# Kernel tuning notes

Hardware: AMD Instinct MI355X
Metric: run time of the kernel (lower is better)

The kernel has to match this reference:

```python
import jax, jax.numpy as jnp
import numpy as np

NUM_HEADS = 4
HEAD_DIM = 64  # hidden_dim // num_heads = 256 // 4
NEG_SLOPE = 0.2


def setup_inputs() -> dict:
    key0 = jax.random.key(0)
    ks = jax.random.split(key0, 8)
    B, N, QD, VD = 32, 8192, 256, 256
    HD = NUM_HEADS * HEAD_DIM  # 256
    s_in = 1.0 / np.sqrt(QD)
    s_v = 1.0 / np.sqrt(VD)
    s_a = 1.0 / np.sqrt(HEAD_DIM)
    return {
        "query": jax.random.normal(ks[0], (B, QD), jnp.float32),
        "key": jax.random.normal(ks[1], (B, N, QD), jnp.float32),
        "value": jax.random.normal(ks[2], (B, N, VD), jnp.float32),
        # linear_query == linear_key (shared_weights=True)
        "Wq": jax.random.uniform(ks[3], (QD, HD), jnp.float32, -s_in, s_in),
        "bq": jax.random.uniform(ks[4], (HD,), jnp.float32, -s_in, s_in),
        # node_projection
        "Wv": jax.random.uniform(ks[5], (VD, HD), jnp.float32, -s_v, s_v),
        "bv": jax.random.uniform(ks[6], (HD,), jnp.float32, -s_v, s_v),
        # attention: Linear(head_dim, 1, bias=False)
        "a": jax.random.uniform(ks[7], (HEAD_DIM,), jnp.float32, -s_a, s_a),
    }


def reference(query, key, value, Wq, bq, Wv, bv, a):
    B, N, _ = key.shape
    H, D = NUM_HEADS, HEAD_DIM
    # projections (shared query/key weights)
    hq = (query @ Wq + bq).reshape(B, 1, H, D)          # [B,1,H,D]
    hk = (key @ Wq + bq).reshape(B, N, H, D)            # [B,N,H,D]
    hv = (value @ Wv + bv).reshape(B, N, H, D)          # [B,N,H,D]
    # additive attention score: leaky_relu(broadcast add) projected to scalar per head
    e = jax.nn.leaky_relu(hq + hk, negative_slope=NEG_SLOPE)  # [B,N,H,D]
    e = jnp.einsum('bnhd,d->bnh', e, a)                 # [B,N,H]
    # dropout=0.0 (eval) -> identity; softmax over nodes
    e = jax.nn.softmax(e, axis=1)                       # [B,N,H]
    scored = jnp.einsum('bnh,bnhf->bhf', e, hv)         # [B,H,D]
    h_prime = jax.nn.relu(scored.reshape(B, H * D))     # [B,H*D] (is_concat)
    return h_prime, e
```

## Files before the change

kernel.cpp:

```cpp
#include <hip/hip_runtime.h>
#include <hip/hip_bf16.h>

#define NUM_HEADS 4
#define HD 256
#define QD 256
#define VD 256
#define B_SZ 32
#define N_NODES 8192
#define NEG_SLOPE 0.2f
#define CH 16
#define NCH 32
#define KSTRIDE 1040

typedef short bf16x8 __attribute__((ext_vector_type(8)));
typedef float f32x4 __attribute__((ext_vector_type(4)));

static __device__ __forceinline__ unsigned short f2bf(float f) {
    __hip_bfloat16 h = __float2bfloat16(f);
    return *reinterpret_cast<unsigned short*>(&h);
}

static __device__ __forceinline__ void gload_lds16(const float* g, void* l) {
    __builtin_amdgcn_global_load_lds(
        (const __attribute__((address_space(1))) void*)g,
        (__attribute__((address_space(3))) void*)l, 16, 0, 0);
}

__global__ __launch_bounds__(256)
void prep_kernel(const float* __restrict__ query,
                 const float* __restrict__ Wq,
                 const float* __restrict__ bq,
                 unsigned short* __restrict__ WqP,
                 float* __restrict__ hqb) {
    int blk = blockIdx.x;
    int tid = threadIdx.x;
    if (blk < 32) {
        int b = blk, col = tid;
        float acc = 2.0f * bq[col];
#pragma unroll 16
        for (int k = 0; k < QD; ++k)
            acc += query[b * QD + k] * Wq[k * HD + col];
        hqb[b * HD + col] = acc;
    } else {
        int idx = blk - 32;
        int kstep = idx >> 2, g = idx & 3;
        int col = tid;
        int h = col >> 6, ct = (col >> 4) & 3, col16 = col & 15;
        unsigned short v[8];
#pragma unroll
        for (int j = 0; j < 8; ++j)
            v[j] = f2bf(Wq[(kstep * 32 + g * 8 + j) * HD + col]);
        *reinterpret_cast<uint4*>(
            WqP + kstep * 8192 + h * 2048 + ct * 512 + (g * 16 + col16) * 8) =
            *reinterpret_cast<uint4*>(v);
    }
}

__global__ __launch_bounds__(256, 2)
void fused_kernel(const float* __restrict__ key,
                  const float* __restrict__ value,
                  const unsigned short* __restrict__ WqP,
                  const float* __restrict__ hqb,
                  const float* __restrict__ avec,
                  float* __restrict__ s,
                  float* __restrict__ p_part,
                  float* __restrict__ pml) {
    __shared__ __align__(16) char smem[2 * (CH * KSTRIDE) + 2 * (CH * 1024)];

    char* kb0 = smem;
    char* kb1 = smem + CH * KSTRIDE;
    char* vb0 = smem + 2 * CH * KSTRIDE;
    char* vb1 = vb0 + CH * 1024;

    int bid = blockIdx.x;
    int b = bid >> 4, strip = bid & 15;
    int tid = threadIdx.x;
    int w = tid >> 6, lane = tid & 63;
    int col16 = lane & 15, g = (lane >> 4) & 3;
    int h = w;
    int rowbase0 = strip * 512;

    bf16x8 bfr[8][4];
    {
        const unsigned short* wp0 = WqP + h * 2048 + (g * 16 + col16) * 8;
#pragma unroll
        for (int ks = 0; ks < 8; ++ks)
#pragma unroll
            for (int ct = 0; ct < 4; ++ct)
                bfr[ks][ct] = *reinterpret_cast<const bf16x8*>(wp0 + ks * 8192 + ct * 512);
    }
    float av16[4][4], hq16[4][4];
#pragma unroll
    for (int ct = 0; ct < 4; ++ct)
#pragma unroll
        for (int r = 0; r < 4; ++r) {
            int d = ct * 16 + g * 4 + r;
            av16[ct][r] = avec[d];
            hq16[ct][r] = hqb[b * HD + h * 64 + d];
        }

    float mr = -1e30f, lr = 0.f;
    f32x4 pa = (f32x4){0.f, 0.f, 0.f, 0.f};

    {
        int rb = rowbase0;
#pragma unroll
        for (int r = 0; r < 4; ++r) {
            int lr_ = w * 4 + r;
            gload_lds16(key + ((size_t)(b * N_NODES + rb + lr_)) * QD + lane * 4,
                        kb0 + lr_ * KSTRIDE);
        }
#pragma unroll
        for (int r = 0; r < 4; ++r) {
            int lr_ = w * 4 + r;
            gload_lds16(value + ((size_t)(b * N_NODES + rb + lr_)) * VD + lane * 4,
                        vb0 + lr_ * 1024);
        }
    }

    for (int t = 0; t < NCH; ++t) {
        __builtin_amdgcn_s_barrier();
        if (t + 1 < NCH) {
            char* kbn = ((t + 1) & 1) ? kb1 : kb0;
            char* vbn = ((t + 1) & 1) ? vb1 : vb0;
            int rb = rowbase0 + (t + 1) * CH;
#pragma unroll
            for (int r = 0; r < 4; ++r) {
                int lr_ = w * 4 + r;
                gload_lds16(key + ((size_t)(b * N_NODES + rb + lr_)) * QD + lane * 4,
                            kbn + lr_ * KSTRIDE);
            }
#pragma unroll
            for (int r = 0; r < 4; ++r) {
                int lr_ = w * 4 + r;
                gload_lds16(value + ((size_t)(b * N_NODES + rb + lr_)) * VD + lane * 4,
                            vbn + lr_ * 1024);
            }
            asm volatile("s_waitcnt vmcnt(8)" ::: "memory");
        } else {
            asm volatile("s_waitcnt vmcnt(0)" ::: "memory");
        }
        __builtin_amdgcn_s_barrier();
        __builtin_amdgcn_sched_barrier(0);

        const char* kb = (t & 1) ? kb1 : kb0;
        const char* vb = (t & 1) ? vb1 : vb0;
        int n0c = rowbase0 + t * CH;

        bf16x8 a[8];
#pragma unroll
        for (int ks = 0; ks < 8; ++ks) {
            f32x4 lo = *reinterpret_cast<const f32x4*>(kb + col16 * KSTRIDE + ks * 128 + g * 32);
            f32x4 hi = *reinterpret_cast<const f32x4*>(kb + col16 * KSTRIDE + ks * 128 + g * 32 + 16);
            unsigned int u0, u1, u2, u3;
            asm("v_cvt_pk_bf16_f32 %0, %1, %2" : "=v"(u0) : "v"(lo[0]), "v"(lo[1]));
            asm("v_cvt_pk_bf16_f32 %0, %1, %2" : "=v"(u1) : "v"(lo[2]), "v"(lo[3]));
            asm("v_cvt_pk_bf16_f32 %0, %1, %2" : "=v"(u2) : "v"(hi[0]), "v"(hi[1]));
            asm("v_cvt_pk_bf16_f32 %0, %1, %2" : "=v"(u3) : "v"(hi[2]), "v"(hi[3]));
            uint4 tt = {u0, u1, u2, u3};
            a[ks] = *reinterpret_cast<bf16x8*>(&tt);
        }

        f32x4 acc[4];
#pragma unroll
        for (int ct = 0; ct < 4; ++ct) acc[ct] = (f32x4){0.f, 0.f, 0.f, 0.f};
#pragma unroll
        for (int ks = 0; ks < 8; ++ks)
#pragma unroll
            for (int ct = 0; ct < 4; ++ct)
                acc[ct] = __builtin_amdgcn_mfma_f32_16x16x32_bf16(bfr[ks][ct], a[ks], acc[ct], 0, 0, 0);

        float dot = 0.f;
#pragma unroll
        for (int ct = 0; ct < 4; ++ct) {
#pragma unroll
            for (int r = 0; r < 4; ++r) {
                float pre = acc[ct][r] + hq16[ct][r];
                float tv = fmaxf(pre, NEG_SLOPE * pre);
                dot += av16[ct][r] * tv;
            }
        }
        dot += __shfl_xor(dot, 16, 64);
        dot += __shfl_xor(dot, 32, 64);

        if (lane < 16) {
            s[((size_t)(b * NUM_HEADS + h)) * N_NODES + n0c + lane] = dot;
        }

        float mc = dot;
        mc = fmaxf(mc, __shfl_xor(mc, 1, 64));
        mc = fmaxf(mc, __shfl_xor(mc, 2, 64));
        mc = fmaxf(mc, __shfl_xor(mc, 4, 64));
        mc = fmaxf(mc, __shfl_xor(mc, 8, 64));
        float mnew = fmaxf(mr, mc);
        float ep = __expf(dot - mnew);
        float lc = ep;
        lc += __shfl_xor(lc, 1, 64);
        lc += __shfl_xor(lc, 2, 64);
        lc += __shfl_xor(lc, 4, 64);
        lc += __shfl_xor(lc, 8, 64);
        float scf = __expf(mr - mnew);
        pa *= scf;
        lr = lr * scf + lc;
        mr = mnew;

#pragma unroll
        for (int n = 0; n < 16; ++n) {
            f32x4 v = *reinterpret_cast<const f32x4*>(vb + n * 1024 + lane * 16);
            float e = __shfl(ep, n, 64);
            pa += e * v;
        }
    }

    int slot = bid * 4 + w;
    *reinterpret_cast<f32x4*>(p_part + (size_t)slot * 256 + lane * 4) = pa;
    if (lane == 0) {
        pml[slot * 2] = mr;
        pml[slot * 2 + 1] = lr;
    }
}

__global__ __launch_bounds__(256)
void final_kernel(const float* __restrict__ p_part,
                  const float* __restrict__ pml,
                  const float* __restrict__ Wv,
                  const float* __restrict__ bv,
                  float* __restrict__ hout,
                  float* __restrict__ sc) {
    int bh = blockIdx.x;
    int b = bh >> 2, h = bh & 3;
    int tid = threadIdx.x;

    int slots[16];
    float mv[16], lv[16];
    float M = -1e30f;
#pragma unroll
    for (int i = 0; i < 16; ++i) {
        slots[i] = (b * 16 + i) * 4 + h;
        mv[i] = pml[slots[i] * 2];
        lv[i] = pml[slots[i] * 2 + 1];
        M = fmaxf(M, mv[i]);
    }
    float L = 0.f, acc = 0.f;
#pragma unroll
    for (int i = 0; i < 16; ++i) {
        float wf = __expf(mv[i] - M);
        L += wf * lv[i];
        acc += wf * p_part[(size_t)slots[i] * 256 + tid];
    }
    float invL = 1.0f / L;
    if (tid == 0) {
        sc[bh * 2] = M;
        sc[bh * 2 + 1] = invL;
    }
    __shared__ float ps[256];
    ps[tid] = acc * invL;
    __syncthreads();

    int d = tid & 63, kr = tid >> 6;
    float a2 = 0.f;
#pragma unroll 8
    for (int k = kr * 64; k < kr * 64 + 64; ++k)
        a2 += ps[k] * Wv[k * HD + h * 64 + d];
    __shared__ float rs[4][64];
    rs[kr][d] = a2;
    __syncthreads();
    if (tid < 64) {
        float o = bv[h * 64 + tid] + rs[0][tid] + rs[1][tid] + rs[2][tid] + rs[3][tid];
        hout[b * HD + h * 64 + tid] = fmaxf(o, 0.f);
    }
}

__global__ __launch_bounds__(256)
void epass_kernel(const float* __restrict__ s,
                  const float* __restrict__ sc,
                  float* __restrict__ e_out) {
    int bid = blockIdx.x;
    int b = bid >> 5, t = bid & 31;
    int n = t * 256 + threadIdx.x;
    float4 ev;
#pragma unroll
    for (int h = 0; h < 4; ++h) {
        float M = sc[(b * 4 + h) * 2];
        float invL = sc[(b * 4 + h) * 2 + 1];
        float sv = s[((size_t)(b * 4 + h)) * N_NODES + n];
        (&ev.x)[h] = __expf(sv - M) * invL;
    }
    *reinterpret_cast<float4*>(e_out + ((size_t)(b * N_NODES + n)) * 4) = ev;
}

extern "C" void kernel_launch(void* const* d_in, const int* in_sizes, int n_in,
                              void* d_out, int out_size, void* d_ws, size_t ws_size,
                              hipStream_t stream) {
    const float* query = (const float*)d_in[0];
    const float* key   = (const float*)d_in[1];
    const float* value = (const float*)d_in[2];
    const float* Wq    = (const float*)d_in[3];
    const float* bq    = (const float*)d_in[4];
    const float* Wv    = (const float*)d_in[5];
    const float* bv    = (const float*)d_in[6];
    const float* avec  = (const float*)d_in[7];
    float* out = (float*)d_out;

    char* ws = (char*)d_ws;
    unsigned short* WqP = (unsigned short*)ws;
    float* hqb    = (float*)(ws + 131072);
    float* s      = (float*)(ws + 163840);
    float* pml    = (float*)(ws + 4358144);
    float* sc     = (float*)(ws + 4374528);
    float* p_part = (float*)(ws + 4378624);

    prep_kernel<<<64, 256, 0, stream>>>(query, Wq, bq, WqP, hqb);
    fused_kernel<<<512, 256, 0, stream>>>(key, value, WqP, hqb, avec, s, p_part, pml);
    final_kernel<<<B_SZ * NUM_HEADS, 256, 0, stream>>>(p_part, pml, Wv, bv, out, sc);
    epass_kernel<<<B_SZ * 32, 256, 0, stream>>>(s, sc, out + B_SZ * HD);
}
```

Measured before the change: 132.3 us.

## Warp-specialize fused kernel with producer loaders and 3-slot LDS ring

The fused kernel now runs 512 threads per block. Four producer waves stream key/value chunks into a 3-slot shared-memory ring, and four consumer waves (one per head) do the MFMA score and online-softmax accumulation. Handoff uses LDS flag counters with atomics and spin-sleep instead of block-wide barriers. Each block covers 1024 nodes, so half as many blocks launch and the final reduction merges 8 partials instead of 16. The goal is to overlap global loads with compute more deeply. The cost is fewer blocks, spin-wait overhead, and the risk that flag ordering bugs produce hazards.

After: 187.4 us. 41.6% more time.

```diff
diff --git a/kernel.cpp b/kernel.cpp
--- a/kernel.cpp
+++ b/kernel.cpp
@@ -9,8 +9,10 @@
 #define N_NODES 8192
 #define NEG_SLOPE 0.2f
 #define CH 16
-#define NCH 32
+#define NCH 64
 #define KSTRIDE 1040
+#define RING 3
+#define SLOT (CH * KSTRIDE + CH * 1024)
 
 typedef short bf16x8 __attribute__((ext_vector_type(8)));
 typedef float f32x4 __attribute__((ext_vector_type(4)));
@@ -56,7 +58,7 @@
     }
 }
 
-__global__ __launch_bounds__(256, 2)
+__global__ __launch_bounds__(512, 2)
 void fused_kernel(const float* __restrict__ key,
                   const float* __restrict__ value,
                   const unsigned short* __restrict__ WqP,
@@ -65,158 +67,154 @@
                   float* __restrict__ s,
                   float* __restrict__ p_part,
                   float* __restrict__ pml) {
-    __shared__ __align__(16) char smem[2 * (CH * KSTRIDE) + 2 * (CH * 1024)];
-
-    char* kb0 = smem;
-    char* kb1 = smem + CH * KSTRIDE;
-    char* vb0 = smem + 2 * CH * KSTRIDE;
-    char* vb1 = vb0 + CH * 1024;
+    __shared__ __align__(16) char smem[RING * SLOT + 64];
+    int* flags = reinterpret_cast<int*>(smem + RING * SLOT);
+    volatile int* vflags = flags;
 
     int bid = blockIdx.x;
-    int b = bid >> 4, strip = bid & 15;
+    int b = bid >> 3, strip = bid & 7;
     int tid = threadIdx.x;
     int w = tid >> 6, lane = tid & 63;
-    int col16 = lane & 15, g = (lane >> 4) & 3;
-    int h = w;
-    int rowbase0 = strip * 512;
-
-    bf16x8 bfr[8][4];
-    {
-        const unsigned short* wp0 = WqP + h * 2048 + (g * 16 + col16) * 8;
-#pragma unroll
-        for (int ks = 0; ks < 8; ++ks)
-#pragma unroll
-            for (int ct = 0; ct < 4; ++ct)
-                bfr[ks][ct] = *reinterpret_cast<const bf16x8*>(wp0 + ks * 8192 + ct * 512);
-    }
-    float av16[4][4], hq16[4][4];
-#pragma unroll
-    for (int ct = 0; ct < 4; ++ct)
-#pragma unroll
-        for (int r = 0; r < 4; ++r) {
-            int d = ct * 16 + g * 4 + r;
-            av16[ct][r] = avec[d];
-            hq16[ct][r] = hqb[b * HD + h * 64 + d];
-        }
-
-    float mr = -1e30f, lr = 0.f;
-    f32x4 pa = (f32x4){0.f, 0.f, 0.f, 0.f};
-
-    {
-        int rb = rowbase0;
-#pragma unroll
-        for (int r = 0; r < 4; ++r) {
-            int lr_ = w * 4 + r;
-            gload_lds16(key + ((size_t)(b * N_NODES + rb + lr_)) * QD + lane * 4,
-                        kb0 + lr_ * KSTRIDE);
-        }
-#pragma unroll
-        for (int r = 0; r < 4; ++r) {
-            int lr_ = w * 4 + r;
-            gload_lds16(value + ((size_t)(b * N_NODES + rb + lr_)) * VD + lane * 4,
-                        vb0 + lr_ * 1024);
-        }
-    }
-
-    for (int t = 0; t < NCH; ++t) {
-        __builtin_amdgcn_s_barrier();
-        if (t + 1 < NCH) {
-            char* kbn = ((t + 1) & 1) ? kb1 : kb0;
-            char* vbn = ((t + 1) & 1) ? vb1 : vb0;
-            int rb = rowbase0 + (t + 1) * CH;
+    int rowbase0 = strip * 1024;
+
+    if (tid < 2 * RING) flags[tid] = (tid < RING) ? 0 : 4;
+    __syncthreads();
+
+    if (w < 4) {
+        for (int t = 0; t < NCH; ++t) {
+            int sl = t % RING, e = t / RING;
+            while (vflags[RING + sl] < 4 * e + 4) __builtin_amdgcn_s_sleep(2);
+            char* kslot = smem + sl * SLOT;
+            char* vslot = kslot + CH * KSTRIDE;
+            int rb = rowbase0 + t * CH;
 #pragma unroll
             for (int r = 0; r < 4; ++r) {
                 int lr_ = w * 4 + r;
                 gload_lds16(key + ((size_t)(b * N_NODES + rb + lr_)) * QD + lane * 4,
-                            kbn + lr_ * KSTRIDE);
+                            kslot + lr_ * KSTRIDE);
             }
 #pragma unroll
             for (int r = 0; r < 4; ++r) {
                 int lr_ = w * 4 + r;
                 gload_lds16(value + ((size_t)(b * N_NODES + rb + lr_)) * VD + lane * 4,
-                            vbn + lr_ * 1024);
-            }
-            asm volatile("s_waitcnt vmcnt(8)" ::: "memory");
-        } else {
-            asm volatile("s_waitcnt vmcnt(0)" ::: "memory");
+                            vslot + lr_ * 1024);
+            }
+            if (t > 0) {
+                asm volatile("s_waitcnt vmcnt(8)" ::: "memory");
+                if (lane == 0) atomicAdd(&flags[(t - 1) % RING], 1);
+            }
         }
-        __builtin_amdgcn_s_barrier();
-        __builtin_amdgcn_sched_barrier(0);
-
-        const char* kb = (t & 1) ? kb1 : kb0;
-        const char* vb = (t & 1) ? vb1 : vb0;
-        int n0c = rowbase0 + t * CH;
-
-        bf16x8 a[8];
-#pragma unroll
-        for (int ks = 0; ks < 8; ++ks) {
-            f32x4 lo = *reinterpret_cast<const f32x4*>(kb + col16 * KSTRIDE + ks * 128 + g * 32);
-            f32x4 hi = *reinterpret_cast<const f32x4*>(kb + col16 * KSTRIDE + ks * 128 + g * 32 + 16);
-            unsigned int u0, u1, u2, u3;
-            asm("v_cvt_pk_bf16_f32 %0, %1, %2" : "=v"(u0) : "v"(lo[0]), "v"(lo[1]));
-            asm("v_cvt_pk_bf16_f32 %0, %1, %2" : "=v"(u1) : "v"(lo[2]), "v"(lo[3]));
-            asm("v_cvt_pk_bf16_f32 %0, %1, %2" : "=v"(u2) : "v"(hi[0]), "v"(hi[1]));
-            asm("v_cvt_pk_bf16_f32 %0, %1, %2" : "=v"(u3) : "v"(hi[2]), "v"(hi[3]));
-            uint4 tt = {u0, u1, u2, u3};
-            a[ks] = *reinterpret_cast<bf16x8*>(&tt);
+        asm volatile("s_waitcnt vmcnt(0)" ::: "memory");
+        if (lane == 0) atomicAdd(&flags[(NCH - 1) % RING], 1);
+    } else {
+        int h = w - 4;
+        int col16 = lane & 15, g = (lane >> 4) & 3;
+
+        bf16x8 bfr[8][4];
+        {
+            const unsigned short* wp0 = WqP + h * 2048 + (g * 16 + col16) * 8;
+#pragma unroll
+            for (int ks = 0; ks < 8; ++ks)
+#pragma unroll
+                for (int ct = 0; ct < 4; ++ct)
+                    bfr[ks][ct] = *reinterpret_cast<const bf16x8*>(wp0 + ks * 8192 + ct * 512);
         }
-
-        f32x4 acc[4];
-#pragma unroll
-        for (int ct = 0; ct < 4; ++ct) acc[ct] = (f32x4){0.f, 0.f, 0.f, 0.f};
-#pragma unroll
-        for (int ks = 0; ks < 8; ++ks)
-#pragma unroll
-            for (int ct = 0; ct < 4; ++ct)
-                acc[ct] = __builtin_amdgcn_mfma_f32_16x16x32_bf16(bfr[ks][ct], a[ks], acc[ct], 0, 0, 0);
-
-        float dot = 0.f;
-#pragma unroll
-        for (int ct = 0; ct < 4; ++ct) {
+        float av16[4][4], hq16[4][4];
+#pragma unroll
+        for (int ct = 0; ct < 4; ++ct)
 #pragma unroll
             for (int r = 0; r < 4; ++r) {
-                float pre = acc[ct][r] + hq16[ct][r];
-                float tv = fmaxf(pre, NEG_SLOPE * pre);
-                dot += av16[ct][r] * tv;
-            }
+                int d = ct * 16 + g * 4 + r;
+                av16[ct][r] = avec[d];
+                hq16[ct][r] = hqb[b * HD + h * 64 + d];
+            }
+
+        float mr = -1e30f, lr = 0.f;
+        f32x4 pa = (f32x4){0.f, 0.f, 0.f, 0.f};
+
+        for (int t = 0; t < NCH; ++t) {
+            int sl = t % RING, e = t / RING;
+            while (vflags[sl] < 4 * (e + 1)) __builtin_amdgcn_s_sleep(2);
+            asm volatile("s_waitcnt lgkmcnt(0)" ::: "memory");
+            __builtin_amdgcn_sched_barrier(0);
+
+            const char* kb = smem + sl * SLOT;
+            const char* vb = kb + CH * KSTRIDE;
+            int n0c = rowbase0 + t * CH;
+
+            bf16x8 a[8];
+#pragma unroll
+            for (int ks = 0; ks < 8; ++ks) {
+                f32x4 lo = *reinterpret_cast<const f32x4*>(kb + col16 * KSTRIDE + ks * 128 + g * 32);
+                f32x4 hi = *reinterpret_cast<const f32x4*>(kb + col16 * KSTRIDE + ks * 128 + g * 32 + 16);
+                unsigned int u0, u1, u2, u3;
+                asm("v_cvt_pk_bf16_f32 %0, %1, %2" : "=v"(u0) : "v"(lo[0]), "v"(lo[1]));
+                asm("v_cvt_pk_bf16_f32 %0, %1, %2" : "=v"(u1) : "v"(lo[2]), "v"(lo[3]));
+                asm("v_cvt_pk_bf16_f32 %0, %1, %2" : "=v"(u2) : "v"(hi[0]), "v"(hi[1]));
+                asm("v_cvt_pk_bf16_f32 %0, %1, %2" : "=v"(u3) : "v"(hi[2]), "v"(hi[3]));
+                uint4 tt = {u0, u1, u2, u3};
+                a[ks] = *reinterpret_cast<bf16x8*>(&tt);
+            }
+
+            f32x4 acc[4];
+#pragma unroll
+            for (int ct = 0; ct < 4; ++ct) acc[ct] = (f32x4){0.f, 0.f, 0.f, 0.f};
+#pragma unroll
+            for (int ks = 0; ks < 8; ++ks)
+#pragma unroll
+                for (int ct = 0; ct < 4; ++ct)
+                    acc[ct] = __builtin_amdgcn_mfma_f32_16x16x32_bf16(bfr[ks][ct], a[ks], acc[ct], 0, 0, 0);
+
+            float dot = 0.f;
+#pragma unroll
+            for (int ct = 0; ct < 4; ++ct) {
+#pragma unroll
+                for (int r = 0; r < 4; ++r) {
+                    float pre = acc[ct][r] + hq16[ct][r];
+                    float tv = fmaxf(pre, NEG_SLOPE * pre);
+                    dot += av16[ct][r] * tv;
+                }
+            }
+            dot += __shfl_xor(dot, 16, 64);
+            dot += __shfl_xor(dot, 32, 64);
+
+            if (lane < 16)
+                s[((size_t)(b * NUM_HEADS + h)) * N_NODES + n0c + lane] = dot;
+
+            float mc = dot;
+            mc = fmaxf(mc, __shfl_xor(mc, 1, 64));
+            mc = fmaxf(mc, __shfl_xor(mc, 2, 64));
+            mc = fmaxf(mc, __shfl_xor(mc, 4, 64));
+            mc = fmaxf(mc, __shfl_xor(mc, 8, 64));
+            float mnew = fmaxf(mr, mc);
+            float ep = __expf(dot - mnew);
+            float lc = ep;
+            lc += __shfl_xor(lc, 1, 64);
+            lc += __shfl_xor(lc, 2, 64);
+            lc += __shfl_xor(lc, 4, 64);
+            lc += __shfl_xor(lc, 8, 64);
+            float scf = __expf(mr - mnew);
+            pa *= scf;
+            lr = lr * scf + lc;
+            mr = mnew;
+
+#pragma unroll
+            for (int n = 0; n < 16; ++n) {
+                f32x4 v = *reinterpret_cast<const f32x4*>(vb + n * 1024 + lane * 16);
+                float e2 = __shfl(ep, n, 64);
+                pa += e2 * v;
+            }
+
+            asm volatile("s_waitcnt lgkmcnt(0)" ::: "memory");
+            if (lane == 0) atomicAdd(&flags[RING + sl], 1);
         }
-        dot += __shfl_xor(dot, 16, 64);
-        dot += __shfl_xor(dot, 32, 64);
-
-        if (lane < 16) {
-            s[((size_t)(b * NUM_HEADS + h)) * N_NODES + n0c + lane] = dot;
+
+        int slot = bid * 4 + h;
+        *reinterpret_cast<f32x4*>(p_part + (size_t)slot * 256 + lane * 4) = pa;
+        if (lane == 0) {
+            pml[slot * 2] = mr;
+            pml[slot * 2 + 1] = lr;
         }
-
-        float mc = dot;
-        mc = fmaxf(mc, __shfl_xor(mc, 1, 64));
-        mc = fmaxf(mc, __shfl_xor(mc, 2, 64));
-        mc = fmaxf(mc, __shfl_xor(mc, 4, 64));
-        mc = fmaxf(mc, __shfl_xor(mc, 8, 64));
-        float mnew = fmaxf(mr, mc);
-        float ep = __expf(dot - mnew);
-        float lc = ep;
-        lc += __shfl_xor(lc, 1, 64);
-        lc += __shfl_xor(lc, 2, 64);
-        lc += __shfl_xor(lc, 4, 64);
-        lc += __shfl_xor(lc, 8, 64);
-        float scf = __expf(mr - mnew);
-        pa *= scf;
-        lr = lr * scf + lc;
-        mr = mnew;
-
-#pragma unroll
-        for (int n = 0; n < 16; ++n) {
-            f32x4 v = *reinterpret_cast<const f32x4*>(vb + n * 1024 + lane * 16);
-            float e = __shfl(ep, n, 64);
-            pa += e * v;
-        }
-    }
-
-    int slot = bid * 4 + w;
-    *reinterpret_cast<f32x4*>(p_part + (size_t)slot * 256 + lane * 4) = pa;
-    if (lane == 0) {
-        pml[slot * 2] = mr;
-        pml[slot * 2 + 1] = lr;
     }
 }
 
@@ -231,19 +229,19 @@
     int b = bh >> 2, h = bh & 3;
     int tid = threadIdx.x;
 
-    int slots[16];
-    float mv[16], lv[16];
+    int slots[8];
+    float mv[8], lv[8];
     float M = -1e30f;
 #pragma unroll
-    for (int i = 0; i < 16; ++i) {
-        slots[i] = (b * 16 + i) * 4 + h;
+    for (int i = 0; i < 8; ++i) {
+        slots[i] = (b * 8 + i) * 4 + h;
         mv[i] = pml[slots[i] * 2];
         lv[i] = pml[slots[i] * 2 + 1];
         M = fmaxf(M, mv[i]);
     }
     float L = 0.f, acc = 0.f;
 #pragma unroll
-    for (int i = 0; i < 16; ++i) {
+    for (int i = 0; i < 8; ++i) {
         float wf = __expf(mv[i] - M);
         L += wf * lv[i];
         acc += wf * p_part[(size_t)slots[i] * 256 + tid];
@@ -307,11 +305,11 @@
     float* hqb    = (float*)(ws + 131072);
     float* s      = (float*)(ws + 163840);
     float* pml    = (float*)(ws + 4358144);
-    float* sc     = (float*)(ws + 4374528);
-    float* p_part = (float*)(ws + 4378624);
+    float* sc     = (float*)(ws + 4390912);
+    float* p_part = (float*)(ws + 4395008);
 
     prep_kernel<<<64, 256, 0, stream>>>(query, Wq, bq, WqP, hqb);
-    fused_kernel<<<512, 256, 0, stream>>>(key, value, WqP, hqb, avec, s, p_part, pml);
+    fused_kernel<<<256, 512, 0, stream>>>(key, value, WqP, hqb, avec, s, p_part, pml);
     final_kernel<<<B_SZ * NUM_HEADS, 256, 0, stream>>>(p_part, pml, Wv, bv, out, sc);
     epass_kernel<<<B_SZ * 32, 256, 0, stream>>>(s, sc, out + B_SZ * HD);
 }
```

## Split each head's columns across two waves using 512-thread blocks

Applied to the files above, without the earlier changes.

Fused kernel now launches 512 threads per block, with 8 waves. Each head's 64 output columns are split across two waves, and each wave also takes half of the 16 rows in the value accumulation. Partial scores are combined through a small shared buffer with an extra __syncthreads per chunk. The final kernel now merges 32 partial softmax states per (batch, head) instead of 16. The aim is more waves in flight and fewer registers per wave to better hide memory latency, at the cost of an extra block barrier per chunk and twice as many partials.

New measurement: 235.1 us. 77.6% more time.

```diff
diff --git a/kernel.cpp b/kernel.cpp
--- a/kernel.cpp
+++ b/kernel.cpp
@@ -56,7 +56,7 @@
     }
 }
 
-__global__ __launch_bounds__(256, 2)
+__global__ __launch_bounds__(512, 4)
 void fused_kernel(const float* __restrict__ key,
                   const float* __restrict__ value,
                   const unsigned short* __restrict__ WqP,
@@ -65,38 +65,38 @@
                   float* __restrict__ s,
                   float* __restrict__ p_part,
                   float* __restrict__ pml) {
-    __shared__ __align__(16) char smem[2 * (CH * KSTRIDE) + 2 * (CH * 1024)];
-
+    __shared__ __align__(16) char smem[2 * (CH * KSTRIDE) + 2 * (CH * 1024) + 512];
     char* kb0 = smem;
     char* kb1 = smem + CH * KSTRIDE;
     char* vb0 = smem + 2 * CH * KSTRIDE;
     char* vb1 = vb0 + CH * 1024;
+    float (*xbuf)[2][16] = reinterpret_cast<float(*)[2][16]>(vb1 + CH * 1024);
 
     int bid = blockIdx.x;
     int b = bid >> 4, strip = bid & 15;
     int tid = threadIdx.x;
     int w = tid >> 6, lane = tid & 63;
     int col16 = lane & 15, g = (lane >> 4) & 3;
-    int h = w;
+    int h = w & 3, cth = w >> 2;
     int rowbase0 = strip * 512;
 
-    bf16x8 bfr[8][4];
+    bf16x8 bfr[8][2];
     {
-        const unsigned short* wp0 = WqP + h * 2048 + (g * 16 + col16) * 8;
+        const unsigned short* wp0 = WqP + h * 2048 + cth * 1024 + (g * 16 + col16) * 8;
 #pragma unroll
         for (int ks = 0; ks < 8; ++ks)
 #pragma unroll
-            for (int ct = 0; ct < 4; ++ct)
-                bfr[ks][ct] = *reinterpret_cast<const bf16x8*>(wp0 + ks * 8192 + ct * 512);
-    }
-    float av16[4][4], hq16[4][4];
-#pragma unroll
-    for (int ct = 0; ct < 4; ++ct)
+            for (int ctl = 0; ctl < 2; ++ctl)
+                bfr[ks][ctl] = *reinterpret_cast<const bf16x8*>(wp0 + ks * 8192 + ctl * 512);
+    }
+    float av8[2][4], hq8[2][4];
+#pragma unroll
+    for (int ctl = 0; ctl < 2; ++ctl)
 #pragma unroll
         for (int r = 0; r < 4; ++r) {
-            int d = ct * 16 + g * 4 + r;
-            av16[ct][r] = avec[d];
-            hq16[ct][r] = hqb[b * HD + h * 64 + d];
+            int d = (cth * 2 + ctl) * 16 + g * 4 + r;
+            av8[ctl][r] = avec[d];
+            hq8[ctl][r] = hqb[b * HD + h * 64 + d];
         }
 
     float mr = -1e30f, lr = 0.f;
@@ -105,14 +105,10 @@
     {
         int rb = rowbase0;
 #pragma unroll
-        for (int r = 0; r < 4; ++r) {
-            int lr_ = w * 4 + r;
+        for (int r = 0; r < 2; ++r) {
+            int lr_ = w * 2 + r;
             gload_lds16(key + ((size_t)(b * N_NODES + rb + lr_)) * QD + lane * 4,
                         kb0 + lr_ * KSTRIDE);
-        }
-#pragma unroll
-        for (int r = 0; r < 4; ++r) {
-            int lr_ = w * 4 + r;
             gload_lds16(value + ((size_t)(b * N_NODES + rb + lr_)) * VD + lane * 4,
                         vb0 + lr_ * 1024);
         }
@@ -125,18 +121,18 @@
             char* vbn = ((t + 1) & 1) ? vb1 : vb0;
             int rb = rowbase0 + (t + 1) * CH;
 #pragma unroll
-            for (int r = 0; r < 4; ++r) {
-                int lr_ = w * 4 + r;
+            for (int r = 0; r < 2; ++r) {
+                int lr_ = w * 2 + r;
                 gload_lds16(key + ((size_t)(b * N_NODES + rb + lr_)) * QD + lane * 4,
                             kbn + lr_ * KSTRIDE);
             }
 #pragma unroll
-            for (int r = 0; r < 4; ++r) {
-                int lr_ = w * 4 + r;
+            for (int r = 0; r < 2; ++r) {
+                int lr_ = w * 2 + r;
                 gload_lds16(value + ((size_t)(b * N_NODES + rb + lr_)) * VD + lane * 4,
                             vbn + lr_ * 1024);
             }
-            asm volatile("s_waitcnt vmcnt(8)" ::: "memory");
+            asm volatile("s_waitcnt vmcnt(4)" ::: "memory");
         } else {
             asm volatile("s_waitcnt vmcnt(0)" ::: "memory");
         }
@@ -147,53 +143,60 @@
         const char* vb = (t & 1) ? vb1 : vb0;
         int n0c = rowbase0 + t * CH;
 
-        bf16x8 a[8];
-#pragma unroll
-        for (int ks = 0; ks < 8; ++ks) {
-            f32x4 lo = *reinterpret_cast<const f32x4*>(kb + col16 * KSTRIDE + ks * 128 + g * 32);
-            f32x4 hi = *reinterpret_cast<const f32x4*>(kb + col16 * KSTRIDE + ks * 128 + g * 32 + 16);
-            unsigned int u0, u1, u2, u3;
-            asm("v_cvt_pk_bf16_f32 %0, %1, %2" : "=v"(u0) : "v"(lo[0]), "v"(lo[1]));
-            asm("v_cvt_pk_bf16_f32 %0, %1, %2" : "=v"(u1) : "v"(lo[2]), "v"(lo[3]));
-            asm("v_cvt_pk_bf16_f32 %0, %1, %2" : "=v"(u2) : "v"(hi[0]), "v"(hi[1]));
-            asm("v_cvt_pk_bf16_f32 %0, %1, %2" : "=v"(u3) : "v"(hi[2]), "v"(hi[3]));
-            uint4 tt = {u0, u1, u2, u3};
-            a[ks] = *reinterpret_cast<bf16x8*>(&tt);
-        }
-
-        f32x4 acc[4];
-#pragma unroll
-        for (int ct = 0; ct < 4; ++ct) acc[ct] = (f32x4){0.f, 0.f, 0.f, 0.f};
-#pragma unroll
-        for (int ks = 0; ks < 8; ++ks)
-#pragma unroll
-            for (int ct = 0; ct < 4; ++ct)
-                acc[ct] = __builtin_amdgcn_mfma_f32_16x16x32_bf16(bfr[ks][ct], a[ks], acc[ct], 0, 0, 0);
-
-        float dot = 0.f;
-#pragma unroll
-        for (int ct = 0; ct < 4; ++ct) {
+        f32x4 acc[2];
+        acc[0] = (f32x4){0.f, 0.f, 0.f, 0.f};
+        acc[1] = acc[0];
+#pragma unroll
+        for (int kh = 0; kh < 2; ++kh) {
+            bf16x8 a[4];
+#pragma unroll
+            for (int k2 = 0; k2 < 4; ++k2) {
+                int ks = kh * 4 + k2;
+                f32x4 lo = *reinterpret_cast<const f32x4*>(kb + col16 * KSTRIDE + ks * 128 + g * 32);
+                f32x4 hi = *reinterpret_cast<const f32x4*>(kb + col16 * KSTRIDE + ks * 128 + g * 32 + 16);
+                unsigned int u0, u1, u2, u3;
+                asm("v_cvt_pk_bf16_f32 %0, %1, %2" : "=v"(u0) : "v"(lo[0]), "v"(lo[1]));
+                asm("v_cvt_pk_bf16_f32 %0, %1, %2" : "=v"(u1) : "v"(lo[2]), "v"(lo[3]));
+                asm("v_cvt_pk_bf16_f32 %0, %1, %2" : "=v"(u2) : "v"(hi[0]), "v"(hi[1]));
+                asm("v_cvt_pk_bf16_f32 %0, %1, %2" : "=v"(u3) : "v"(hi[2]), "v"(hi[3]));
+                uint4 tt = {u0, u1, u2, u3};
+                a[k2] = *reinterpret_cast<bf16x8*>(&tt);
+            }
+#pragma unroll
+            for (int k2 = 0; k2 < 4; ++k2)
+#pragma unroll
+                for (int ctl = 0; ctl < 2; ++ctl)
+                    acc[ctl] = __builtin_amdgcn_mfma_f32_16x16x32_bf16(
+                        bfr[kh * 4 + k2][ctl], a[k2], acc[ctl], 0, 0, 0);
+        }
+
+        float dp = 0.f;
+#pragma unroll
+        for (int ctl = 0; ctl < 2; ++ctl)
 #pragma unroll
             for (int r = 0; r < 4; ++r) {
-                float pre = acc[ct][r] + hq16[ct][r];
+                float pre = acc[ctl][r] + hq8[ctl][r];
                 float tv = fmaxf(pre, NEG_SLOPE * pre);
-                dot += av16[ct][r] * tv;
+                dp += av8[ctl][r] * tv;
             }
-        }
-        dot += __shfl_xor(dot, 16, 64);
-        dot += __shfl_xor(dot, 32, 64);
-
-        if (lane < 16) {
-            s[((size_t)(b * NUM_HEADS + h)) * N_NODES + n0c + lane] = dot;
-        }
-
-        float mc = dot;
+        dp += __shfl_xor(dp, 16, 64);
+        dp += __shfl_xor(dp, 32, 64);
+
+        if (lane < 16) xbuf[h][cth][col16] = dp;
+        __syncthreads();
+        float pfull = dp + xbuf[h][1 - cth][col16];
+
+        if (cth == 0 && lane < 16)
+            s[((size_t)(b * NUM_HEADS + h)) * N_NODES + n0c + lane] = pfull;
+
+        float mydot = ((col16 >> 3) == cth) ? pfull : -1e30f;
+        float mc = mydot;
         mc = fmaxf(mc, __shfl_xor(mc, 1, 64));
         mc = fmaxf(mc, __shfl_xor(mc, 2, 64));
         mc = fmaxf(mc, __shfl_xor(mc, 4, 64));
         mc = fmaxf(mc, __shfl_xor(mc, 8, 64));
         float mnew = fmaxf(mr, mc);
-        float ep = __expf(dot - mnew);
+        float ep = __expf(mydot - mnew);
         float lc = ep;
         lc += __shfl_xor(lc, 1, 64);
         lc += __shfl_xor(lc, 2, 64);
@@ -205,14 +208,15 @@
         mr = mnew;
 
 #pragma unroll
-        for (int n = 0; n < 16; ++n) {
-            f32x4 v = *reinterpret_cast<const f32x4*>(vb + n * 1024 + lane * 16);
-            float e = __shfl(ep, n, 64);
+        for (int n = 0; n < 8; ++n) {
+            int row = cth * 8 + n;
+            f32x4 v = *reinterpret_cast<const f32x4*>(vb + row * 1024 + lane * 16);
+            float e = __shfl(ep, row, 64);
             pa += e * v;
         }
     }
 
-    int slot = bid * 4 + w;
+    int slot = bid * 8 + cth * 4 + h;
     *reinterpret_cast<f32x4*>(p_part + (size_t)slot * 256 + lane * 4) = pa;
     if (lane == 0) {
         pml[slot * 2] = mr;
@@ -231,22 +235,19 @@
     int b = bh >> 2, h = bh & 3;
     int tid = threadIdx.x;
 
-    int slots[16];
-    float mv[16], lv[16];
     float M = -1e30f;
-#pragma unroll
-    for (int i = 0; i < 16; ++i) {
-        slots[i] = (b * 16 + i) * 4 + h;
-        mv[i] = pml[slots[i] * 2];
-        lv[i] = pml[slots[i] * 2 + 1];
-        M = fmaxf(M, mv[i]);
+#pragma unroll 8
+    for (int i = 0; i < 32; ++i) {
+        int slot = (b * 16 + (i >> 1)) * 8 + (i & 1) * 4 + h;
+        M = fmaxf(M, pml[slot * 2]);
     }
     float L = 0.f, acc = 0.f;
-#pragma unroll
-    for (int i = 0; i < 16; ++i) {
-        float wf = __expf(mv[i] - M);
-        L += wf * lv[i];
-        acc += wf * p_part[(size_t)slots[i] * 256 + tid];
+#pragma unroll 8
+    for (int i = 0; i < 32; ++i) {
+        int slot = (b * 16 + (i >> 1)) * 8 + (i & 1) * 4 + h;
+        float wf = __expf(pml[slot * 2] - M);
+        L += wf * pml[slot * 2 + 1];
+        acc += wf * p_part[(size_t)slot * 256 + tid];
     }
     float invL = 1.0f / L;
     if (tid == 0) {
@@ -307,11 +308,11 @@
     float* hqb    = (float*)(ws + 131072);
     float* s      = (float*)(ws + 163840);
     float* pml    = (float*)(ws + 4358144);
-    float* sc     = (float*)(ws + 4374528);
-    float* p_part = (float*)(ws + 4378624);
+    float* sc     = (float*)(ws + 4390912);
+    float* p_part = (float*)(ws + 4395008);
 
     prep_kernel<<<64, 256, 0, stream>>>(query, Wq, bq, WqP, hqb);
-    fused_kernel<<<512, 256, 0, stream>>>(key, value, WqP, hqb, avec, s, p_part, pml);
+    fused_kernel<<<512, 512, 0, stream>>>(key, value, WqP, hqb, avec, s, p_part, pml);
     final_kernel<<<B_SZ * NUM_HEADS, 256, 0, stream>>>(p_part, pml, Wv, bv, out, sc);
     epass_kernel<<<B_SZ * 32, 256, 0, stream>>>(s, sc, out + B_SZ * HD);
 }
```
